# Kernel optimization log

Hardware: AMD Instinct MI355X
Metric: run time of the kernel (lower is better)

## Reference

```python
import math
import jax, jax.numpy as jnp
import numpy as np

D = 4  # BWGNN d


def calculate_theta2(d):
    # Faithful numeric reimplementation of the sympy version.
    # f_i(x) = (x/2)^i (1-x/2)^(d-i) / (2*Beta(i+1, d+1-i)); the original code
    # keeps only the d lowest-order (ascending) coefficients, dropping x^d.
    thetas = []
    for i in range(d):
        c1 = np.zeros(i + 1); c1[i] = 0.5 ** i                      # (x/2)^i
        c2 = np.array([math.comb(d - i, j) * (-0.5) ** j
                       for j in range(d - i + 1)])                   # (1-x/2)^(d-i)
        c = np.convolve(c1, c2)                                      # ascending, len d+1
        B = math.factorial(i) * math.factorial(d - i) / math.factorial(d + 1)
        c = c / (2.0 * B)
        thetas.append([float(c[j]) for j in range(d)])               # coeff[d-i] slicing
    return thetas

THETAS = calculate_theta2(D)


def setup_inputs() -> dict:
    key = jax.random.key(0)
    k1, k2, k3, k4 = jax.random.split(key, 4)
    N, E, F_in, H = 100000, 1600000, 128, 64
    feature = jax.random.normal(k1, (N, F_in), dtype=jnp.float32)
    edge_index = jax.random.randint(k2, (2, E), 0, N, dtype=jnp.int32)
    W = jax.random.normal(k3, (F_in, H), dtype=jnp.float32) * 0.05
    b = jax.random.normal(k4, (H,), dtype=jnp.float32) * 0.05
    return {"feature": feature, "edge_index": edge_index, "W": W, "b": b}


def reference(feature, edge_index, W, b):
    N = feature.shape[0]
    src, dst = edge_index[0], edge_index[1]
    # out_degrees: number of out-edges per node (src side), clamped to >= 1
    deg = jax.ops.segment_sum(jnp.ones_like(src, dtype=jnp.float32), src,
                              num_segments=N)
    D_invsqrt = jnp.maximum(deg, 1.0) ** -0.5  # [N]
    D_invsqrt = D_invsqrt[:, None]             # [N,1]

    h = jax.nn.leaky_relu(feature @ W + b, negative_slope=0.01)  # [N,H]

    def unn_laplacian(feat):
        # feat - D^{-1/2} A^T D^{-1/2} feat  (copy_u + sum over dst)
        msg = (feat * D_invsqrt)[src]                          # [E,H]
        agg = jax.ops.segment_sum(msg, dst, num_segments=N)    # [N,H]
        return feat - agg * D_invsqrt

    outs = []
    for theta in THETAS:
        feat = h
        acc = theta[0] * feat
        for k in range(1, len(theta)):
            feat = unn_laplacian(feat)
            acc = acc + theta[k] * feat
        outs.append(acc)
    return jnp.concatenate(outs, axis=1)  # [N, len(THETAS)*H]
```

## Files before the change

### kernel.cpp

```cpp
#include <hip/hip_runtime.h>

#define THREADS 256
#define T1 4096
#define BCAP 8192
#define NBMAX 512

__device__ __forceinline__ float bf2f(unsigned short u) {
    return __uint_as_float(((unsigned int)u) << 16);
}
__device__ __forceinline__ unsigned short f2bf(float x) {
    unsigned int u = __float_as_uint(x);
    u += 0x7fffu + ((u >> 16) & 1u);
    return (unsigned short)(u >> 16);
}
__device__ __forceinline__ float blo(unsigned int x) { return __uint_as_float(x << 16); }
__device__ __forceinline__ float bhi(unsigned int x) { return __uint_as_float(x & 0xffff0000u); }

__global__ void zero_kernel(int* __restrict__ p, int n) {
    const int i = blockIdx.x * blockDim.x + threadIdx.x;
    if (i < n) p[i] = 0;
}

__global__ void bin_kernel(const int* __restrict__ src, const int* __restrict__ dst,
                           int* __restrict__ gFillD, unsigned int* __restrict__ gBufD,
                           int* __restrict__ gFillS, unsigned int* __restrict__ gBufS,
                           int E, int tiles) {
    __shared__ int cnt[NBMAX], scanB[NBMAX], gbase[NBMAX], place[NBMAX];
    __shared__ unsigned int stage[T1], addr[T1];
    const int tid = threadIdx.x;
    const bool isS = blockIdx.x >= tiles;
    const int tile = isS ? blockIdx.x - tiles : blockIdx.x;
    const int* key = isS ? src : dst;
    int* gFill = isS ? gFillS : gFillD;
    unsigned int* gBuf = isS ? gBufS : gBufD;
    const int tileStart = tile * T1;
    const int tileCnt = min(T1, E - tileStart);

    for (int i = tid; i < NBMAX; i += THREADS) { cnt[i] = 0; place[i] = 0; }
    __syncthreads();

    for (int i = tid; i < tileCnt; i += THREADS)
        atomicAdd(&cnt[key[tileStart + i] >> 8], 1);
    __syncthreads();

    if (tid < 64) {
        const int base = tid * 8;
        int loc[8]; int s = 0;
        #pragma unroll
        for (int k = 0; k < 8; ++k) { loc[k] = s; s += cnt[base + k]; }
        int run = s;
        #pragma unroll
        for (int off = 1; off < 64; off <<= 1) {
            int t = __shfl_up(run, off);
            if (tid >= off) run += t;
        }
        const int excl = run - s;
        #pragma unroll
        for (int k = 0; k < 8; ++k) scanB[base + k] = excl + loc[k];
    }
    __syncthreads();

    for (int i = tid; i < NBMAX; i += THREADS)
        gbase[i] = atomicAdd(&gFill[i], cnt[i]);
    __syncthreads();

    for (int i = tid; i < tileCnt; i += THREADS) {
        const int kk = key[tileStart + i];
        const int b = kk >> 8;
        const unsigned int rec = isS ? (unsigned int)(kk & 255)
                                     : (((unsigned int)(kk & 255) << 17) | (unsigned int)src[tileStart + i]);
        const int pos = atomicAdd(&place[b], 1);
        const int li = scanB[b] + pos;
        const int gi = gbase[b] + pos;
        stage[li] = rec;
        addr[li] = (gi < BCAP) ? (unsigned int)(b * BCAP + gi) : 0xFFFFFFFFu;
    }
    __syncthreads();

    for (int i = tid; i < tileCnt; i += THREADS) {
        const unsigned int a = addr[i];
        if (a != 0xFFFFFFFFu) gBuf[a] = stage[i];
    }
}

__global__ void scanb_kernel(const int* __restrict__ gFill, int* __restrict__ gBase,
                             int* __restrict__ rowptr, int nb, int N) {
    __shared__ int s[NBMAX];
    const int tid = threadIdx.x;
    const int v = (tid < nb) ? min(gFill[tid], BCAP) : 0;
    s[tid] = v;
    __syncthreads();
    for (int off = 1; off < NBMAX; off <<= 1) {
        int t = (tid >= off) ? s[tid - off] : 0;
        __syncthreads();
        s[tid] += t;
        __syncthreads();
    }
    if (tid < nb) gBase[tid] = s[tid] - v;
    if (tid == NBMAX - 1) rowptr[N] = s[NBMAX - 1];
}

__global__ void csr_kernel(const int* __restrict__ gFill, const int* __restrict__ gBase,
                           const unsigned int* __restrict__ gBuf,
                           int* __restrict__ rowptr, int* __restrict__ col, int N) {
    __shared__ int fillT[256], offT[256], place[256], sc[256];
    __shared__ int colT[BCAP];
    __shared__ int nwrite;
    const int tid = threadIdx.x;
    const int b = blockIdx.x;
    const int nrec = min(gFill[b], BCAP);
    const int base = gBase[b];

    fillT[tid] = 0; place[tid] = 0;
    __syncthreads();
    for (int i = tid; i < nrec; i += THREADS)
        atomicAdd(&fillT[gBuf[(size_t)b * BCAP + i] >> 17], 1);
    __syncthreads();

    int v = fillT[tid];
    sc[tid] = v;
    __syncthreads();
    for (int off = 1; off < 256; off <<= 1) {
        int t = (tid >= off) ? sc[tid - off] : 0;
        __syncthreads();
        sc[tid] += t;
        __syncthreads();
    }
    offT[tid] = sc[tid] - v;
    if (tid == 255) nwrite = sc[255];
    __syncthreads();

    const int node0 = b << 8;
    const int nvalid = min(256, N - node0);
    if (tid < nvalid) rowptr[node0 + tid] = base + offT[tid];

    for (int i = tid; i < nrec; i += THREADS) {
        const unsigned int rec = gBuf[(size_t)b * BCAP + i];
        const int dlow = rec >> 17;
        const int s = rec & 0x1FFFF;
        const int pos = atomicAdd(&place[dlow], 1);
        colT[offT[dlow] + pos] = s;
    }
    __syncthreads();

    const int nw = nwrite;
    for (int i = tid; i < nw; i += THREADS) col[base + i] = colT[i];
}

__global__ void deg_kernel2(const int* __restrict__ gFill, const unsigned int* __restrict__ gBuf,
                            int* __restrict__ deg, int N) {
    __shared__ int cntT[256];
    const int tid = threadIdx.x;
    const int b = blockIdx.x;
    const int nrec = min(gFill[b], BCAP);
    for (int i = tid; i < 256; i += THREADS) cntT[i] = 0;
    __syncthreads();
    for (int i = tid; i < nrec; i += THREADS)
        atomicAdd(&cntT[gBuf[(size_t)b * BCAP + i] & 255], 1);
    __syncthreads();
    const int node0 = b << 8;
    const int nvalid = min(256, N - node0);
    for (int t = tid; t < nvalid; t += THREADS) deg[node0 + t] = cntT[t];
}

__global__ void count_fb(const int* __restrict__ src, const int* __restrict__ dst,
                         int* __restrict__ deg, int* __restrict__ cntd, int E) {
    const int stride = gridDim.x * blockDim.x;
    for (int i = blockIdx.x * blockDim.x + threadIdx.x; i < E; i += stride) {
        atomicAdd(&deg[src[i]], 1);
        atomicAdd(&cntd[dst[i]], 1);
    }
}
__global__ void scan_fb(const int* __restrict__ cnt, int* __restrict__ rowptr, int N) {
    __shared__ int s[256];
    __shared__ int carry;
    const int tid = threadIdx.x;
    if (tid == 0) carry = 0;
    __syncthreads();
    for (int basei = 0; basei < N; basei += 256) {
        const int i = basei + tid;
        const int v = (i < N) ? cnt[i] : 0;
        s[tid] = v;
        __syncthreads();
        for (int off = 1; off < 256; off <<= 1) {
            int t = (tid >= off) ? s[tid - off] : 0;
            __syncthreads();
            s[tid] += t;
            __syncthreads();
        }
        if (i < N) rowptr[i] = carry + s[tid] - v;
        __syncthreads();
        if (tid == 0) carry += s[255];
        __syncthreads();
    }
    if (tid == 0) rowptr[N] = carry;
}
__global__ void fill_fb(const int* __restrict__ src, const int* __restrict__ dst,
                        const int* __restrict__ rowptr, int* __restrict__ place,
                        int* __restrict__ col, int E) {
    const int stride = gridDim.x * blockDim.x;
    for (int i = blockIdx.x * blockDim.x + threadIdx.x; i < E; i += stride) {
        const int d = dst[i];
        col[rowptr[d] + atomicAdd(&place[d], 1)] = src[i];
    }
}

__global__ void gemm_leaky(const float* __restrict__ feat, const float* __restrict__ W,
                           const float* __restrict__ b, const int* __restrict__ deg,
                           unsigned short* __restrict__ S0, int N) {
    __shared__ float Wl[128 * 64];
    __shared__ float fl[64][132];
    __shared__ float bl[64];

    {
        const float4* W4 = (const float4*)W;
        float4* Wl4 = (float4*)Wl;
        for (int i = threadIdx.x; i < 2048; i += THREADS) Wl4[i] = W4[i];
        if (threadIdx.x < 64) bl[threadIdx.x] = b[threadIdx.x];
    }

    const int cg = threadIdx.x & 15;
    const int rg = threadIdx.x >> 4;
    const int ntiles = (N + 63) >> 6;

    for (int tile = blockIdx.x; tile < ntiles; tile += gridDim.x) {
        const int n0 = tile << 6;
        __syncthreads();
        for (int i = threadIdx.x; i < 2048; i += THREADS) {
            int rr = i >> 5;
            int kk = i & 31;
            float4 v = make_float4(0.f, 0.f, 0.f, 0.f);
            if (n0 + rr < N) v = ((const float4*)(feat + (size_t)(n0 + rr) * 128))[kk];
            *((float4*)&fl[rr][kk * 4]) = v;
        }
        __syncthreads();

        float acc[4][4];
        #pragma unroll
        for (int j = 0; j < 4; ++j) {
            float bv = bl[cg * 4 + j];
            acc[0][j] = bv; acc[1][j] = bv; acc[2][j] = bv; acc[3][j] = bv;
        }

        #pragma unroll 4
        for (int k = 0; k < 128; ++k) {
            const float4 w = *((const float4*)&Wl[k * 64 + cg * 4]);
            const float f0 = fl[rg * 4 + 0][k];
            const float f1 = fl[rg * 4 + 1][k];
            const float f2 = fl[rg * 4 + 2][k];
            const float f3 = fl[rg * 4 + 3][k];
            acc[0][0] += f0 * w.x; acc[0][1] += f0 * w.y; acc[0][2] += f0 * w.z; acc[0][3] += f0 * w.w;
            acc[1][0] += f1 * w.x; acc[1][1] += f1 * w.y; acc[1][2] += f1 * w.z; acc[1][3] += f1 * w.w;
            acc[2][0] += f2 * w.x; acc[2][1] += f2 * w.y; acc[2][2] += f2 * w.z; acc[2][3] += f2 * w.w;
            acc[3][0] += f3 * w.x; acc[3][1] += f3 * w.y; acc[3][2] += f3 * w.z; acc[3][3] += f3 * w.w;
        }

        #pragma unroll
        for (int i = 0; i < 4; ++i) {
            const int n = n0 + rg * 4 + i;
            if (n < N) {
                const float dv = rsqrtf(fmaxf((float)deg[n], 1.0f));
                ushort4 o;
                float v0 = acc[i][0] > 0.f ? acc[i][0] : 0.01f * acc[i][0];
                float v1 = acc[i][1] > 0.f ? acc[i][1] : 0.01f * acc[i][1];
                float v2 = acc[i][2] > 0.f ? acc[i][2] : 0.01f * acc[i][2];
                float v3 = acc[i][3] > 0.f ? acc[i][3] : 0.01f * acc[i][3];
                o.x = f2bf(v0 * dv); o.y = f2bf(v1 * dv); o.z = f2bf(v2 * dv); o.w = f2bf(v3 * dv);
                *((ushort4*)(S0 + (size_t)n * 64 + cg * 4)) = o;
            }
        }
    }
}

template<bool FINAL>
__global__ void hop_kernel(const int* __restrict__ rowptr, const int* __restrict__ col,
                           const int* __restrict__ deg,
                           const unsigned short* __restrict__ Sprev,
                           unsigned short* __restrict__ Snext,
                           const unsigned short* __restrict__ S0,
                           const unsigned short* __restrict__ S1,
                           float* __restrict__ out, int N) {
    const int lane = threadIdx.x & 63;
    const int g = lane >> 3;
    const int q = lane & 7;
    const int nwaves = (gridDim.x * blockDim.x) >> 6;
    for (int n = (blockIdx.x * blockDim.x + threadIdx.x) >> 6; n < N; n += nwaves) {
        const int beg = rowptr[n];
        const int end = rowptr[n + 1];
        float a[8];
        #pragma unroll
        for (int k = 0; k < 8; ++k) a[k] = 0.f;

        for (int e0 = beg; e0 < end; e0 += 64) {
            const int idx = e0 + lane;
            const int c = (idx < end) ? col[idx] : 0;
            const int m = min(64, end - e0);
            for (int j = 0; j < m; j += 8) {
                const int jg = j + g;
                const int s = __shfl(c, jg & 63);
                if (jg < m) {
                    const uint4 u = *(const uint4*)(Sprev + (size_t)s * 64 + q * 8);
                    a[0] += blo(u.x); a[1] += bhi(u.x);
                    a[2] += blo(u.y); a[3] += bhi(u.y);
                    a[4] += blo(u.z); a[5] += bhi(u.z);
                    a[6] += blo(u.w); a[7] += bhi(u.w);
                }
            }
        }
        #pragma unroll
        for (int k = 0; k < 8; ++k) {
            a[k] += __shfl_xor(a[k], 8);
            a[k] += __shfl_xor(a[k], 16);
            a[k] += __shfl_xor(a[k], 32);
        }

        const float d = fmaxf((float)deg[n], 1.0f);
        const float inv = 1.0f / d;
        const uint4 uo = *(const uint4*)(Sprev + (size_t)n * 64 + q * 8);
        float own[8], sn[8];
        own[0] = blo(uo.x); own[1] = bhi(uo.x); own[2] = blo(uo.y); own[3] = bhi(uo.y);
        own[4] = blo(uo.z); own[5] = bhi(uo.z); own[6] = blo(uo.w); own[7] = bhi(uo.w);
        #pragma unroll
        for (int k = 0; k < 8; ++k) sn[k] = own[k] - a[k] * inv;

        if (!FINAL) {
            if (g == 0) {
                uint4 w;
                w.x = (unsigned int)f2bf(sn[0]) | ((unsigned int)f2bf(sn[1]) << 16);
                w.y = (unsigned int)f2bf(sn[2]) | ((unsigned int)f2bf(sn[3]) << 16);
                w.z = (unsigned int)f2bf(sn[4]) | ((unsigned int)f2bf(sn[5]) << 16);
                w.w = (unsigned int)f2bf(sn[6]) | ((unsigned int)f2bf(sn[7]) << 16);
                *((uint4*)(Snext + (size_t)n * 64 + q * 8)) = w;
            }
        } else if (g < 4) {
            const float sc = sqrtf(d);
            const uint4 u0 = *(const uint4*)(S0 + (size_t)n * 64 + q * 8);
            const uint4 u1 = *(const uint4*)(S1 + (size_t)n * 64 + q * 8);
            float h[8], p1[8];
            h[0] = blo(u0.x); h[1] = bhi(u0.x); h[2] = blo(u0.y); h[3] = bhi(u0.y);
            h[4] = blo(u0.z); h[5] = bhi(u0.z); h[6] = blo(u0.w); h[7] = bhi(u0.w);
            p1[0] = blo(u1.x); p1[1] = bhi(u1.x); p1[2] = blo(u1.y); p1[3] = bhi(u1.y);
            p1[4] = blo(u1.z); p1[5] = bhi(u1.z); p1[6] = blo(u1.w); p1[7] = bhi(u1.w);
            float c0, c1, c2, c3;
            if (g == 0)      { c0 = 2.5f; c1 = -5.0f; c2 = 3.75f;  c3 = -1.25f; }
            else if (g == 1) { c0 = 0.f;  c1 = 5.0f;  c2 = -7.5f;  c3 = 3.75f;  }
            else if (g == 2) { c0 = 0.f;  c1 = 0.f;   c2 = 3.75f;  c3 = -3.75f; }
            else             { c0 = 0.f;  c1 = 0.f;   c2 = 0.f;    c3 = 1.25f;  }
            float o[8];
            #pragma unroll
            for (int k = 0; k < 8; ++k) {
                const float hv = h[k] * sc, p1v = p1[k] * sc, p2v = own[k] * sc, p3v = sn[k] * sc;
                o[k] = c0 * hv + c1 * p1v + c2 * p2v + c3 * p3v;
            }
            float* op = out + (size_t)n * 256 + g * 64 + q * 8;
            *((float4*)op)       = make_float4(o[0], o[1], o[2], o[3]);
            *((float4*)(op + 4)) = make_float4(o[4], o[5], o[6], o[7]);
        }
    }
}

extern "C" void kernel_launch(void* const* d_in, const int* in_sizes, int n_in,
                              void* d_out, int out_size, void* d_ws, size_t ws_size,
                              hipStream_t stream) {
    const float* feature = (const float*)d_in[0];
    const int*   eidx    = (const int*)d_in[1];
    const float* W       = (const float*)d_in[2];
    const float* b       = (const float*)d_in[3];
    float* out = (float*)d_out;

    const int N = in_sizes[0] / 128;
    const int E = in_sizes[1] / 2;
    const int* src = eidx;
    const int* dst = eidx + E;

    const int nb = (N + 255) >> 8;

    int* deg    = (int*)d_ws;
    int* fill   = deg + N;
    int* rowptr = fill + N;
    int* col    = rowptr + (N + 1);
    int* gFillD = col + E;
    int* gFillS = gFillD + NBMAX;
    int* gBase  = gFillS + NBMAX;
    unsigned int* gBufD = (unsigned int*)(gBase + NBMAX);
    unsigned int* gBufS = gBufD + (size_t)nb * BCAP;
    unsigned short* S0 = (unsigned short*)(((uintptr_t)(gBufS + (size_t)nb * BCAP) + 255) & ~(uintptr_t)255);
    unsigned short* S1 = S0 + (size_t)N * 64;
    unsigned short* S2 = S1 + (size_t)N * 64;

    if (N <= 131072) {
        zero_kernel<<<(2 * NBMAX + THREADS - 1) / THREADS, THREADS, 0, stream>>>(gFillD, 2 * NBMAX);
        const int tiles = (E + T1 - 1) / T1;
        bin_kernel<<<2 * tiles, THREADS, 0, stream>>>(src, dst, gFillD, gBufD, gFillS, gBufS, E, tiles);
        scanb_kernel<<<1, NBMAX, 0, stream>>>(gFillD, gBase, rowptr, nb, N);
        csr_kernel<<<nb, THREADS, 0, stream>>>(gFillD, gBase, gBufD, rowptr, col, N);
        deg_kernel2<<<nb, THREADS, 0, stream>>>(gFillS, gBufS, deg, N);
    } else {
        zero_kernel<<<(2 * N + THREADS - 1) / THREADS, THREADS, 0, stream>>>(deg, 2 * N);
        count_fb<<<2048, THREADS, 0, stream>>>(src, dst, deg, fill, E);
        scan_fb<<<1, 256, 0, stream>>>(fill, rowptr, N);
        zero_kernel<<<(N + THREADS - 1) / THREADS, THREADS, 0, stream>>>(fill, N);
        fill_fb<<<2048, THREADS, 0, stream>>>(src, dst, rowptr, fill, col, E);
    }

    const int gemm_blocks = (N + 63) / 64;
    gemm_leaky<<<gemm_blocks, THREADS, 0, stream>>>(feature, W, b, deg, S0, N);

    const int gblocks = (N + 3) / 4;
    hop_kernel<false><<<gblocks, THREADS, 0, stream>>>(rowptr, col, deg, S0, S1, S0, S0, out, N);
    hop_kernel<false><<<gblocks, THREADS, 0, stream>>>(rowptr, col, deg, S1, S2, S0, S0, out, N);
    hop_kernel<true ><<<gblocks, THREADS, 0, stream>>>(rowptr, col, deg, S2, S2, S0, S1, out, N);
}
```

Before: 244.7 us.

## Fuse degree count into CSR build, transpose GEMM tile, unroll hop gathers

The separate degree-count kernel is folded into the CSR build kernel, which reuses its shared histogram to count src-side records for its own node block. This removes one launch and a second pass over the block. The GEMM feature tile is stored transposed in shared memory so each thread reads its four rows with a single float4 load per k. The transposing scatter store is strided and may cause bank conflicts. The hop gather loop now issues two independent neighbour row loads per iteration, giving more memory-level parallelism at some register cost.

Result: faster. 234.2 us (-4.3%).

```diff
diff --git a/kernel.cpp b/kernel.cpp
--- a/kernel.cpp
+++ b/kernel.cpp
@@ -100,21 +100,23 @@
     if (tid == NBMAX - 1) rowptr[N] = s[NBMAX - 1];
 }
 
-__global__ void csr_kernel(const int* __restrict__ gFill, const int* __restrict__ gBase,
-                           const unsigned int* __restrict__ gBuf,
-                           int* __restrict__ rowptr, int* __restrict__ col, int N) {
+__global__ void csr_kernel(const int* __restrict__ gFillD, const int* __restrict__ gBase,
+                           const unsigned int* __restrict__ gBufD,
+                           const int* __restrict__ gFillS, const unsigned int* __restrict__ gBufS,
+                           int* __restrict__ rowptr, int* __restrict__ col,
+                           int* __restrict__ deg, int N) {
     __shared__ int fillT[256], offT[256], place[256], sc[256];
     __shared__ int colT[BCAP];
     __shared__ int nwrite;
     const int tid = threadIdx.x;
     const int b = blockIdx.x;
-    const int nrec = min(gFill[b], BCAP);
+    const int nrec = min(gFillD[b], BCAP);
     const int base = gBase[b];
 
     fillT[tid] = 0; place[tid] = 0;
     __syncthreads();
     for (int i = tid; i < nrec; i += THREADS)
-        atomicAdd(&fillT[gBuf[(size_t)b * BCAP + i] >> 17], 1);
+        atomicAdd(&fillT[gBufD[(size_t)b * BCAP + i] >> 17], 1);
     __syncthreads();
 
     int v = fillT[tid];
@@ -135,7 +137,7 @@
     if (tid < nvalid) rowptr[node0 + tid] = base + offT[tid];
 
     for (int i = tid; i < nrec; i += THREADS) {
-        const unsigned int rec = gBuf[(size_t)b * BCAP + i];
+        const unsigned int rec = gBufD[(size_t)b * BCAP + i];
         const int dlow = rec >> 17;
         const int s = rec & 0x1FFFF;
         const int pos = atomicAdd(&place[dlow], 1);
@@ -145,22 +147,14 @@
 
     const int nw = nwrite;
     for (int i = tid; i < nw; i += THREADS) col[base + i] = colT[i];
-}
-
-__global__ void deg_kernel2(const int* __restrict__ gFill, const unsigned int* __restrict__ gBuf,
-                            int* __restrict__ deg, int N) {
-    __shared__ int cntT[256];
-    const int tid = threadIdx.x;
-    const int b = blockIdx.x;
-    const int nrec = min(gFill[b], BCAP);
-    for (int i = tid; i < 256; i += THREADS) cntT[i] = 0;
-    __syncthreads();
-    for (int i = tid; i < nrec; i += THREADS)
-        atomicAdd(&cntT[gBuf[(size_t)b * BCAP + i] & 255], 1);
-    __syncthreads();
-    const int node0 = b << 8;
-    const int nvalid = min(256, N - node0);
-    for (int t = tid; t < nvalid; t += THREADS) deg[node0 + t] = cntT[t];
+
+    fillT[tid] = 0;
+    __syncthreads();
+    const int nrecS = min(gFillS[b], BCAP);
+    for (int i = tid; i < nrecS; i += THREADS)
+        atomicAdd(&fillT[gBufS[(size_t)b * BCAP + i] & 255], 1);
+    __syncthreads();
+    if (tid < nvalid) deg[node0 + tid] = fillT[tid];
 }
 
 __global__ void count_fb(const int* __restrict__ src, const int* __restrict__ dst,
@@ -209,7 +203,7 @@
                            const float* __restrict__ b, const int* __restrict__ deg,
                            unsigned short* __restrict__ S0, int N) {
     __shared__ float Wl[128 * 64];
-    __shared__ float fl[64][132];
+    __shared__ float fl_t[128][65];
     __shared__ float bl[64];
 
     {
@@ -227,11 +221,14 @@
         const int n0 = tile << 6;
         __syncthreads();
         for (int i = threadIdx.x; i < 2048; i += THREADS) {
-            int rr = i >> 5;
-            int kk = i & 31;
+            const int rr = i >> 5;
+            const int kk = i & 31;
             float4 v = make_float4(0.f, 0.f, 0.f, 0.f);
             if (n0 + rr < N) v = ((const float4*)(feat + (size_t)(n0 + rr) * 128))[kk];
-            *((float4*)&fl[rr][kk * 4]) = v;
+            fl_t[kk * 4 + 0][rr] = v.x;
+            fl_t[kk * 4 + 1][rr] = v.y;
+            fl_t[kk * 4 + 2][rr] = v.z;
+            fl_t[kk * 4 + 3][rr] = v.w;
         }
         __syncthreads();
 
@@ -245,14 +242,11 @@
         #pragma unroll 4
         for (int k = 0; k < 128; ++k) {
             const float4 w = *((const float4*)&Wl[k * 64 + cg * 4]);
-            const float f0 = fl[rg * 4 + 0][k];
-            const float f1 = fl[rg * 4 + 1][k];
-            const float f2 = fl[rg * 4 + 2][k];
-            const float f3 = fl[rg * 4 + 3][k];
-            acc[0][0] += f0 * w.x; acc[0][1] += f0 * w.y; acc[0][2] += f0 * w.z; acc[0][3] += f0 * w.w;
-            acc[1][0] += f1 * w.x; acc[1][1] += f1 * w.y; acc[1][2] += f1 * w.z; acc[1][3] += f1 * w.w;
-            acc[2][0] += f2 * w.x; acc[2][1] += f2 * w.y; acc[2][2] += f2 * w.z; acc[2][3] += f2 * w.w;
-            acc[3][0] += f3 * w.x; acc[3][1] += f3 * w.y; acc[3][2] += f3 * w.z; acc[3][3] += f3 * w.w;
+            const float4 f = *((const float4*)&fl_t[k][rg * 4]);
+            acc[0][0] += f.x * w.x; acc[0][1] += f.x * w.y; acc[0][2] += f.x * w.z; acc[0][3] += f.x * w.w;
+            acc[1][0] += f.y * w.x; acc[1][1] += f.y * w.y; acc[1][2] += f.y * w.z; acc[1][3] += f.y * w.w;
+            acc[2][0] += f.z * w.x; acc[2][1] += f.z * w.y; acc[2][2] += f.z * w.z; acc[2][3] += f.z * w.w;
+            acc[3][0] += f.w * w.x; acc[3][1] += f.w * w.y; acc[3][2] += f.w * w.z; acc[3][3] += f.w * w.w;
         }
 
         #pragma unroll
@@ -295,15 +289,27 @@
             const int idx = e0 + lane;
             const int c = (idx < end) ? col[idx] : 0;
             const int m = min(64, end - e0);
-            for (int j = 0; j < m; j += 8) {
-                const int jg = j + g;
-                const int s = __shfl(c, jg & 63);
-                if (jg < m) {
-                    const uint4 u = *(const uint4*)(Sprev + (size_t)s * 64 + q * 8);
-                    a[0] += blo(u.x); a[1] += bhi(u.x);
-                    a[2] += blo(u.y); a[3] += bhi(u.y);
-                    a[4] += blo(u.z); a[5] += bhi(u.z);
-                    a[6] += blo(u.w); a[7] += bhi(u.w);
+            for (int j = 0; j < m; j += 16) {
+                const int jg0 = j + g;
+                const int jg1 = j + 8 + g;
+                const int s0 = __shfl(c, jg0 & 63);
+                const int s1 = __shfl(c, jg1 & 63);
+                const bool v0 = jg0 < m;
+                const bool v1 = jg1 < m;
+                uint4 u0, u1;
+                if (v0) u0 = *(const uint4*)(Sprev + (size_t)s0 * 64 + q * 8);
+                if (v1) u1 = *(const uint4*)(Sprev + (size_t)s1 * 64 + q * 8);
+                if (v0) {
+                    a[0] += blo(u0.x); a[1] += bhi(u0.x);
+                    a[2] += blo(u0.y); a[3] += bhi(u0.y);
+                    a[4] += blo(u0.z); a[5] += bhi(u0.z);
+                    a[6] += blo(u0.w); a[7] += bhi(u0.w);
+                }
+                if (v1) {
+                    a[0] += blo(u1.x); a[1] += bhi(u1.x);
+                    a[2] += blo(u1.y); a[3] += bhi(u1.y);
+                    a[4] += blo(u1.z); a[5] += bhi(u1.z);
+                    a[6] += blo(u1.w); a[7] += bhi(u1.w);
                 }
             }
         }
@@ -393,8 +399,7 @@
         const int tiles = (E + T1 - 1) / T1;
         bin_kernel<<<2 * tiles, THREADS, 0, stream>>>(src, dst, gFillD, gBufD, gFillS, gBufS, E, tiles);
         scanb_kernel<<<1, NBMAX, 0, stream>>>(gFillD, gBase, rowptr, nb, N);
-        csr_kernel<<<nb, THREADS, 0, stream>>>(gFillD, gBase, gBufD, rowptr, col, N);
-        deg_kernel2<<<nb, THREADS, 0, stream>>>(gFillS, gBufS, deg, N);
+        csr_kernel<<<nb, THREADS, 0, stream>>>(gFillD, gBase, gBufD, gFillS, gBufS, rowptr, col, deg, N);
     } else {
         zero_kernel<<<(2 * N + THREADS - 1) / THREADS, THREADS, 0, stream>>>(deg, 2 * N);
         count_fb<<<2048, THREADS, 0, stream>>>(src, dst, deg, fill, E);
```
